# Performance work log

Hardware: AMD Instinct MI355X
Metric: run time of the kernel (lower is better)

## Reference

```python
import jax, jax.numpy as jnp
import numpy as np

NE = 200000   # num_entities
NR = 16       # num_relations
D  = 128      # embed_dim
B  = 4096     # batch
S  = 64       # neighbors per node
L  = 2        # num_layers
H  = 4        # attention heads (hardcoded in module)


def _ln(x, g, b, eps=1e-5):
    m = jnp.mean(x, -1, keepdims=True)
    v = jnp.mean((x - m) ** 2, -1, keepdims=True)
    return (x - m) * jax.lax.rsqrt(v + eps) * g + b


def setup_inputs() -> dict:
    key = jax.random.key(0)
    ks = jax.random.split(key, 12)
    s = 0.05
    return {
        'drug_entity_indices': jax.random.randint(ks[0], (B,), 0, NE),
        'adj_entity': jax.random.randint(ks[1], (B, S), 0, NE),
        'adj_relation': jax.random.randint(ks[2], (B, S), 0, NR),
        'edge_weights': jax.random.uniform(ks[3], (B, S), dtype=jnp.float32),
        'entity_emb': jax.random.normal(ks[4], (NE, D), jnp.float32) * s,
        'W_rgcn': jax.random.normal(ks[5], (L, NR, D, D), jnp.float32) * s,
        'res_w': jax.random.normal(ks[6], (L, D, D), jnp.float32) * s,
        'res_b': jnp.zeros((L, D), jnp.float32),
        'proj_w': jax.random.normal(ks[7], (L, D, D), jnp.float32) * s,
        'proj_b': jnp.zeros((L, D), jnp.float32),
        'ln_g': jnp.ones((L, D), jnp.float32),
        'ln_b': jnp.zeros((L, D), jnp.float32),
        'in_proj_w': jax.random.normal(ks[8], (3 * D, D), jnp.float32) * s,
        'in_proj_b': jnp.zeros((3 * D,), jnp.float32),
        'out_proj_w': jax.random.normal(ks[9], (D, D), jnp.float32) * s,
        'out_proj_b': jnp.zeros((D,), jnp.float32),
        'fln_g': jnp.ones((D,), jnp.float32),
        'fln_b': jnp.zeros((D,), jnp.float32),
    }


def reference(drug_entity_indices, adj_entity, adj_relation, edge_weights,
              entity_emb, W_rgcn, res_w, res_b, proj_w, proj_b, ln_g, ln_b,
              in_proj_w, in_proj_b, out_proj_w, out_proj_b, fln_g, fln_b):
    node = entity_emb[drug_entity_indices]           # [B,D] combined_emb
    nbr = entity_emb[adj_entity]                     # [B,S,D]
    # Route each edge to its relation: sum_s nbr*ew*[rel==r] then one GEMM per relation
    # (mathematically identical to the per-relation masked matmul loop in torch).
    onehot = jax.nn.one_hot(adj_relation, NR, dtype=node.dtype)      # [B,S,R]
    pre = jnp.einsum('bsd,bsr->brd', nbr * edge_weights[..., None], onehot)
    outs = []
    for l in range(L):
        msgs = jnp.einsum('brd,rde->be', pre, W_rgcn[l])             # [B,D]
        h = jax.nn.relu(node + msgs + node @ res_w[l].T + res_b[l])  # RGCNAggregator
        node = _ln(h @ proj_w[l].T + proj_b[l] + node, ln_g[l], ln_b[l])
        outs.append(node)
    x = jnp.stack(outs, 0)                           # [L,B,D] seq-first
    qkv = x @ in_proj_w.T + in_proj_b
    q, k, v = jnp.split(qkv, 3, axis=-1)
    hd = D // H
    def heads(t):
        return t.reshape(L, B, H, hd).transpose(1, 2, 0, 3)          # [B,H,L,hd]
    q, k, v = heads(q), heads(k), heads(v)
    att = jax.nn.softmax(jnp.einsum('bhld,bhmd->bhlm', q, k) / np.sqrt(hd).astype(np.float32), axis=-1)
    o = jnp.einsum('bhlm,bhmd->bhld', att, v).transpose(2, 0, 1, 3).reshape(L, B, D)
    o = o @ out_proj_w.T + out_proj_b
    return _ln(o.mean(0), fln_g, fln_b)              # [B,D]
```

## Files before the change

kernel.cpp:

```cpp
#include <hip/hip_runtime.h>
#include <math.h>

#define NRREL 16
#define DDIM 128
#define BBATCH 4096
#define SNBR 64
#define ROWS 16

typedef __attribute__((ext_vector_type(8))) short short8;
typedef __attribute__((ext_vector_type(4))) float floatx4;

__device__ __forceinline__ unsigned short f2bf(float f) {
    unsigned u = __builtin_bit_cast(unsigned, f);
    u += 0x7fffu + ((u >> 16) & 1u);
    return (unsigned short)(u >> 16);
}
__device__ __forceinline__ float bf2f(unsigned short u) {
    return __builtin_bit_cast(float, ((unsigned)u) << 16);
}

extern "C" __global__ __launch_bounds__(256)
void k_prep(const float* __restrict__ W_rgcn,
            const float* __restrict__ res_w, const float* __restrict__ proj_w,
            const float* __restrict__ in_w, const float* __restrict__ out_w,
            unsigned short* __restrict__ Wcat, unsigned short* __restrict__ resw,
            unsigned short* __restrict__ projw, unsigned short* __restrict__ inw,
            unsigned short* __restrict__ outw)
{
    __shared__ float tileT[64 * 65];
    const int bid = blockIdx.x, t = threadIdx.x;

    if (bid < 128) {
        const int l = bid >> 6, rem = bid & 63;
        const int k0 = (rem >> 1) * 64, e0 = (rem & 1) * 64;
        #pragma unroll
        for (int i = 0; i < 4; ++i) {
            int flat = t + 256 * i;
            int k = flat >> 4, c = flat & 15;
            float4 v = *(const float4*)(W_rgcn + ((size_t)(l * 2048 + k0 + k)) * 128 + e0 + 4 * c);
            tileT[(4 * c + 0) * 65 + k] = v.x;
            tileT[(4 * c + 1) * 65 + k] = v.y;
            tileT[(4 * c + 2) * 65 + k] = v.z;
            tileT[(4 * c + 3) * 65 + k] = v.w;
        }
        __syncthreads();
        const int e = t >> 2, m = t & 3;
        #pragma unroll
        for (int half = 0; half < 2; ++half) {
            int kk = 16 * m + 8 * half;
            short8 o;
            #pragma unroll
            for (int j = 0; j < 8; ++j) o[j] = (short)f2bf(tileT[e * 65 + kk + j]);
            *(short8*)(Wcat + ((size_t)(l * 128 + e0 + e)) * 2048 + k0 + kk) = o;
        }
    } else {
        int j4 = ((bid - 128) * 256 + t) * 4;
        const float* src; unsigned short* dst; int off;
        if (j4 < 32768)       { src = res_w;  dst = resw;  off = j4; }
        else if (j4 < 65536)  { src = proj_w; dst = projw; off = j4 - 32768; }
        else if (j4 < 114688) { src = in_w;   dst = inw;   off = j4 - 65536; }
        else                  { src = out_w;  dst = outw;  off = j4 - 114688; }
        float4 v = *(const float4*)(src + off);
        ushort4 o = { f2bf(v.x), f2bf(v.y), f2bf(v.z), f2bf(v.w) };
        *(ushort4*)(dst + off) = o;
    }
}

extern "C" __global__ __launch_bounds__(1024)
void k_fused(const int* __restrict__ drug, const int* __restrict__ adj_e,
             const int* __restrict__ adj_r, const float* __restrict__ ew,
             const float* __restrict__ emb,
             const unsigned short* __restrict__ Wcat,
             const unsigned short* __restrict__ resw, const unsigned short* __restrict__ projw,
             const float* __restrict__ res_b, const float* __restrict__ proj_b,
             const float* __restrict__ ln_g, const float* __restrict__ ln_b,
             const unsigned short* __restrict__ inw, const float* __restrict__ in_b,
             const unsigned short* __restrict__ outw, const float* __restrict__ out_b,
             const float* __restrict__ fg, const float* __restrict__ fb,
             float* __restrict__ outp)
{
    __shared__ union {
        struct { unsigned short preA[ROWS * 2056]; } a;
        struct {
            unsigned short h_b16[ROWS * 136];
            unsigned short xs_l[2 * ROWS * 136];
            unsigned short qkvl[2 * ROWS * 392];
        } t;
    } sm;
    __shared__ float node_ln[ROWS * 132];
    __shared__ unsigned short node_b16[ROWS * 136];
    __shared__ union {
        struct {
            int   cnt[ROWS][16];
            int   strt[ROWS][16];
            int   sperm[ROWS][64];
            float wperm[ROWS][64];
        } g;
        float msum[ROWS * 260];
    } sg;
    __shared__ float psum[16][16], psq[16][16];

    const int t = threadIdx.x, w = t >> 6, lane = t & 63, l15 = lane & 15, q = lane >> 4;
    const int r0 = blockIdx.x * ROWS;

    const int erow = t >> 6, es = t & 63;
    int   ent0 = adj_e[(r0 + erow) * SNBR + es];
    float ewt0 = ew[(r0 + erow) * SNBR + es];
    int   rel0 = adj_r[(r0 + erow) * SNBR + es];
    if (t < 256) sg.g.cnt[t >> 4][t & 15] = 0;
    if (t < 512) {
        int rr = t >> 5, c = t & 31;
        int di = drug[r0 + rr];
        float4 v = *(const float4*)(emb + (size_t)di * DDIM + 4 * c);
        *(float4*)(node_ln + rr * 132 + 4 * c) = v;
        ushort4 o = { f2bf(v.x), f2bf(v.y), f2bf(v.z), f2bf(v.w) };
        *(ushort4*)(node_b16 + rr * 136 + 4 * c) = o;
    }
    __syncthreads();

    atomicAdd(&sg.g.cnt[erow][rel0], 1);
    __syncthreads();

    if (t < ROWS) {
        int a = 0;
        #pragma unroll
        for (int r = 0; r < NRREL; ++r) { sg.g.strt[t][r] = a; a += sg.g.cnt[t][r]; }
    }
    __syncthreads();

    {
        int pos0 = atomicAdd(&sg.g.strt[erow][rel0], 1);
        sg.g.sperm[erow][pos0] = ent0;
        sg.g.wperm[erow][pos0] = ewt0;
    }
    __syncthreads();

    {
        #pragma unroll 1
        for (int i = 0; i < 4; ++i) {
            int u = t + 1024 * i;
            int row = u >> 8, rl = (u >> 4) & 15, g8 = u & 15;
            int n = sg.g.cnt[row][rl];
            int end = sg.g.strt[row][rl];
            int beg = end - n;
            float acc[8] = {0.f, 0.f, 0.f, 0.f, 0.f, 0.f, 0.f, 0.f};
            #pragma unroll 1
            for (int jb = beg; jb < end; jb += 8) {
                const float* pp[8]; float wq[8];
                #pragma unroll
                for (int u2 = 0; u2 < 8; ++u2) {
                    int live = (jb + u2 < end);
                    int j = live ? jb + u2 : beg;
                    wq[u2] = live ? sg.g.wperm[row][j] : 0.f;
                    pp[u2] = emb + (size_t)sg.g.sperm[row][j] * DDIM + 8 * g8;
                }
                float4 v0[8], v1[8];
                #pragma unroll
                for (int u2 = 0; u2 < 8; ++u2) {
                    v0[u2] = *(const float4*)pp[u2];
                    v1[u2] = *(const float4*)(pp[u2] + 4);
                }
                #pragma unroll
                for (int u2 = 0; u2 < 8; ++u2) {
                    acc[0] = fmaf(v0[u2].x, wq[u2], acc[0]); acc[1] = fmaf(v0[u2].y, wq[u2], acc[1]);
                    acc[2] = fmaf(v0[u2].z, wq[u2], acc[2]); acc[3] = fmaf(v0[u2].w, wq[u2], acc[3]);
                    acc[4] = fmaf(v1[u2].x, wq[u2], acc[4]); acc[5] = fmaf(v1[u2].y, wq[u2], acc[5]);
                    acc[6] = fmaf(v1[u2].z, wq[u2], acc[6]); acc[7] = fmaf(v1[u2].w, wq[u2], acc[7]);
                }
            }
            short8 o;
            #pragma unroll
            for (int jj = 0; jj < 8; ++jj) o[jj] = (short)f2bf(acc[jj]);
            *(short8*)(sm.a.preA + row * 2056 + rl * DDIM + 8 * g8) = o;
        }
    }
    __syncthreads();

    {
        floatx4 macc = {};
        const unsigned short* ap = sm.a.preA + l15 * 2056 + 8 * q;
        const unsigned short* bp = Wcat + (size_t)(16 * w + l15) * 2048 + 8 * q;
        #pragma unroll 8
        for (int k = 0; k < 2048; k += 32) {
            short8 A = *(const short8*)(ap + k);
            short8 B = *(const short8*)(bp + k);
            macc = __builtin_amdgcn_mfma_f32_16x16x32_bf16(A, B, macc, 0, 0, 0);
        }
        int gc = 16 * w + l15;
        #pragma unroll
        for (int r = 0; r < 4; ++r)
            sg.msum[(4 * q + r) * 260 + gc] = macc[r];
    }
    __syncthreads();

    for (int l = 0; l < 2; ++l) {
        if (w < 8) {
            const unsigned short* Bw = resw + (size_t)l * DDIM * DDIM;
            floatx4 acc = {};
            const unsigned short* ap = node_b16 + l15 * 136 + 8 * q;
            #pragma unroll
            for (int kk = 0; kk < DDIM; kk += 32) {
                short8 A = *(const short8*)(ap + kk);
                short8 B = *(const short8*)(Bw + (size_t)(16 * w + l15) * DDIM + kk + 8 * q);
                acc = __builtin_amdgcn_mfma_f32_16x16x32_bf16(A, B, acc, 0, 0, 0);
            }
            int gc = 16 * w + l15;
            float rb = res_b[l * DDIM + gc];
            #pragma unroll
            for (int r = 0; r < 4; ++r) {
                int lr = 4 * q + r;
                float v = acc[r] + rb + node_ln[lr * 132 + gc] + sg.msum[lr * 260 + l * DDIM + gc];
                sm.t.h_b16[lr * 136 + gc] = f2bf(v > 0.f ? v : 0.f);
            }
        }
        __syncthreads();
        {
            float vv[4];
            int gc = 16 * w + l15;
            if (w < 8) {
                const unsigned short* Bw = projw + (size_t)l * DDIM * DDIM;
                floatx4 acc = {};
                const unsigned short* ap = sm.t.h_b16 + l15 * 136 + 8 * q;
                #pragma unroll
                for (int kk = 0; kk < DDIM; kk += 32) {
                    short8 A = *(const short8*)(ap + kk);
                    short8 B = *(const short8*)(Bw + (size_t)(16 * w + l15) * DDIM + kk + 8 * q);
                    acc = __builtin_amdgcn_mfma_f32_16x16x32_bf16(A, B, acc, 0, 0, 0);
                }
                float s4[4], sq4[4];
                float pb = proj_b[l * DDIM + gc];
                #pragma unroll
                for (int r = 0; r < 4; ++r) {
                    float v = acc[r] + pb + node_ln[(4 * q + r) * 132 + gc];
                    vv[r] = v; s4[r] = v; sq4[r] = v * v;
                }
                #pragma unroll
                for (int r = 0; r < 4; ++r)
                    #pragma unroll
                    for (int off2 = 8; off2 >= 1; off2 >>= 1) {
                        s4[r] += __shfl_xor(s4[r], off2, 64);
                        sq4[r] += __shfl_xor(sq4[r], off2, 64);
                    }
                if (l15 == 0) {
                    #pragma unroll
                    for (int r = 0; r < 4; ++r) {
                        psum[w][4 * q + r] = s4[r];
                        psq[w][4 * q + r] = sq4[r];
                    }
                }
            }
            __syncthreads();
            if (w < 8) {
                float g2 = ln_g[l * DDIM + gc], bb = ln_b[l * DDIM + gc];
                #pragma unroll
                for (int r = 0; r < 4; ++r) {
                    int lr = 4 * q + r;
                    float ssum = 0.f, ssq = 0.f;
                    #pragma unroll
                    for (int ww = 0; ww < 8; ++ww) { ssum += psum[ww][lr]; ssq += psq[ww][lr]; }
                    float mean = ssum * (1.f / DDIM);
                    float var = ssq * (1.f / DDIM) - mean * mean;
                    float val = (vv[r] - mean) * rsqrtf(var + 1e-5f) * g2 + bb;
                    node_ln[lr * 132 + gc] = val;
                    unsigned short ub = f2bf(val);
                    node_b16[lr * 136 + gc] = ub;
                    sm.t.xs_l[(2 * lr + l) * 136 + gc] = ub;
                }
            }
            __syncthreads();
        }
    }

    if (w < 12) {
        floatx4 acc[4] = {};
        const unsigned short* ap = sm.t.xs_l + (16 * (w & 1) + l15) * 136 + 8 * q;
        #pragma unroll
        for (int kk = 0; kk < DDIM; kk += 32) {
            short8 A = *(const short8*)(ap + kk);
            #pragma unroll
            for (int ni = 0; ni < 4; ++ni) {
                short8 B = *(const short8*)(inw + (size_t)(64 * (w >> 1) + ni * 16 + l15) * DDIM + kk + 8 * q);
                acc[ni] = __builtin_amdgcn_mfma_f32_16x16x32_bf16(A, B, acc[ni], 0, 0, 0);
            }
        }
        #pragma unroll
        for (int ni = 0; ni < 4; ++ni) {
            int gc = 64 * (w >> 1) + ni * 16 + l15;
            float ib = in_b[gc];
            #pragma unroll
            for (int r = 0; r < 4; ++r)
                sm.t.qkvl[(16 * (w & 1) + 4 * q + r) * 392 + gc] = f2bf(acc[ni][r] + ib);
        }
    }
    __syncthreads();

    if (t < 128) {
        int g4 = t >> 3, j = t & 7;
        const unsigned short* row0 = sm.t.qkvl + (2 * g4) * 392;
        const unsigned short* row1 = row0 + 392;
        float p00 = 0.f, p01 = 0.f, p10 = 0.f, p11 = 0.f;
        #pragma unroll
        for (int dd = 0; dd < 16; ++dd) {
            int d = 16 * j + dd;
            float q0 = bf2f(row0[d]), k0 = bf2f(row0[128 + d]);
            float q1 = bf2f(row1[d]), k1 = bf2f(row1[128 + d]);
            p00 = fmaf(q0, k0, p00); p01 = fmaf(q0, k1, p01);
            p10 = fmaf(q1, k0, p10); p11 = fmaf(q1, k1, p11);
        }
        p00 += __shfl_xor(p00, 1, 64); p01 += __shfl_xor(p01, 1, 64);
        p10 += __shfl_xor(p10, 1, 64); p11 += __shfl_xor(p11, 1, 64);
        const float sc = 0.17677669529663687f;
        p00 *= sc; p01 *= sc; p10 *= sc; p11 *= sc;
        float m0 = fmaxf(p00, p01), e00 = expf(p00 - m0), e01 = expf(p01 - m0);
        float i0 = 1.f / (e00 + e01);
        float m1 = fmaxf(p10, p11), e10 = expf(p10 - m1), e11 = expf(p11 - m1);
        float i1 = 1.f / (e10 + e11);
        #pragma unroll
        for (int dd = 0; dd < 16; ++dd) {
            int d = 16 * j + dd;
            float v0 = bf2f(row0[256 + d]), v1 = bf2f(row1[256 + d]);
            sm.t.xs_l[(2 * g4) * 136 + d]     = f2bf((e00 * v0 + e01 * v1) * i0);
            sm.t.xs_l[(2 * g4 + 1) * 136 + d] = f2bf((e10 * v0 + e11 * v1) * i1);
        }
    }
    __syncthreads();

    {
        floatx4 acc = {};
        const unsigned short* ap = sm.t.xs_l + (16 * (w & 1) + l15) * 136 + 8 * q;
        #pragma unroll
        for (int kk = 0; kk < DDIM; kk += 32) {
            short8 A = *(const short8*)(ap + kk);
            short8 B = *(const short8*)(outw + (size_t)(16 * (w >> 1) + l15) * DDIM + kk + 8 * q);
            acc = __builtin_amdgcn_mfma_f32_16x16x32_bf16(A, B, acc, 0, 0, 0);
        }
        int gc = 16 * (w >> 1) + l15;
        float ob = out_b[gc];
        float av[2];
        float s2[2], sq2[2];
        #pragma unroll
        for (int rr = 0; rr < 2; ++rr) {
            float v = 0.5f * (acc[2 * rr] + acc[2 * rr + 1]) + ob;
            av[rr] = v; s2[rr] = v; sq2[rr] = v * v;
        }
        #pragma unroll
        for (int rr = 0; rr < 2; ++rr)
            #pragma unroll
            for (int off2 = 8; off2 >= 1; off2 >>= 1) {
                s2[rr] += __shfl_xor(s2[rr], off2, 64);
                sq2[rr] += __shfl_xor(sq2[rr], off2, 64);
            }
        if (l15 == 0) {
            #pragma unroll
            for (int rr = 0; rr < 2; ++rr) {
                psum[w][2 * q + rr] = s2[rr];
                psq[w][2 * q + rr] = sq2[rr];
            }
        }
        __syncthreads();
        float g2 = fg[gc], bb = fb[gc];
        #pragma unroll
        for (int rr = 0; rr < 2; ++rr) {
            int idx = 2 * q + rr;
            float ssum = 0.f, ssq = 0.f;
            #pragma unroll
            for (int ww = 0; ww < 8; ++ww) {
                ssum += psum[2 * ww + (w & 1)][idx];
                ssq  += psq[2 * ww + (w & 1)][idx];
            }
            float mean = ssum * (1.f / DDIM);
            float var = ssq * (1.f / DDIM) - mean * mean;
            outp[(size_t)(r0 + 8 * (w & 1) + idx) * DDIM + gc] =
                (av[rr] - mean) * rsqrtf(var + 1e-5f) * g2 + bb;
        }
    }
}

extern "C" void kernel_launch(void* const* d_in, const int* in_sizes, int n_in,
                              void* d_out, int out_size, void* d_ws, size_t ws_size,
                              hipStream_t stream) {
    const int*   drug_idx = (const int*)d_in[0];
    const int*   adj_ent  = (const int*)d_in[1];
    const int*   adj_rel  = (const int*)d_in[2];
    const float* ew       = (const float*)d_in[3];
    const float* emb      = (const float*)d_in[4];
    const float* W_rgcn   = (const float*)d_in[5];
    const float* res_w    = (const float*)d_in[6];
    const float* res_b    = (const float*)d_in[7];
    const float* proj_w   = (const float*)d_in[8];
    const float* proj_b   = (const float*)d_in[9];
    const float* ln_g     = (const float*)d_in[10];
    const float* ln_b     = (const float*)d_in[11];
    const float* in_w     = (const float*)d_in[12];
    const float* in_b     = (const float*)d_in[13];
    const float* out_w    = (const float*)d_in[14];
    const float* out_b    = (const float*)d_in[15];
    const float* fg       = (const float*)d_in[16];
    const float* fb       = (const float*)d_in[17];
    float* outp = (float*)d_out;

    char* ws = (char*)d_ws;
    size_t off = 0;
    auto alloc = [&](size_t bytes) { size_t o = off; off = (off + bytes + 255) & ~(size_t)255; return o; };
    unsigned short* Wcat    = (unsigned short*)(ws + alloc((size_t)256 * 2048 * 2));
    unsigned short* resw    = (unsigned short*)(ws + alloc((size_t)2 * 128 * 128 * 2));
    unsigned short* projw   = (unsigned short*)(ws + alloc((size_t)2 * 128 * 128 * 2));
    unsigned short* inw     = (unsigned short*)(ws + alloc((size_t)384 * 128 * 2));
    unsigned short* outw    = (unsigned short*)(ws + alloc((size_t)128 * 128 * 2));

    hipLaunchKernelGGL(k_prep, dim3(256), dim3(256), 0, stream,
                       W_rgcn, res_w, proj_w, in_w, out_w,
                       Wcat, resw, projw, inw, outw);
    hipLaunchKernelGGL(k_fused, dim3(BBATCH / ROWS), dim3(1024), 0, stream,
                       drug_idx, adj_ent, adj_rel, ew, emb,
                       Wcat, resw, projw, res_b, proj_b, ln_g, ln_b,
                       inw, in_b, outw, out_b, fg, fb, outp);
}
```

Measured before the change: 232.9 us.

## Restructure neighbor gather so one wave streams a row's sorted edges

The relation-bucketed gather is rebuilt. Previously each thread handled an 8-column slice of one (row, relation) bucket, with variable trip counts and 8-wide batches padded with dead loads. Now each wave owns one row and walks all 64 relation-sorted edges in order. Every lane loads a float2 of each neighbor, with software prefetch of the next 4, and resets its running sum whenever the relation changes. Partial sums are written to LDS at each step so the last write per relation wins, and empty relations are zeroed separately. This aims to remove load imbalance and divergent loops. The cost is narrower 8-byte loads per lane and many redundant LDS stores.

```diff
diff --git a/kernel.cpp b/kernel.cpp
--- a/kernel.cpp
+++ b/kernel.cpp
@@ -95,6 +95,7 @@
             int   strt[ROWS][16];
             int   sperm[ROWS][64];
             float wperm[ROWS][64];
+            int   relperm[ROWS][64];
         } g;
         float msum[ROWS * 260];
     } sg;
@@ -130,48 +131,85 @@
 
     {
         int pos0 = atomicAdd(&sg.g.strt[erow][rel0], 1);
-        sg.g.sperm[erow][pos0] = ent0;
-        sg.g.wperm[erow][pos0] = ewt0;
+        sg.g.sperm[erow][pos0]   = ent0;
+        sg.g.wperm[erow][pos0]   = ewt0;
+        sg.g.relperm[erow][pos0] = rel0;
     }
     __syncthreads();
 
     {
+        const int row = w;
+        if (t < 256) {
+            int rr = t >> 4, rl = t & 15;
+            if (sg.g.cnt[rr][rl] == 0) {
+                short8 z = {};
+                #pragma unroll
+                for (int ii = 0; ii < 16; ++ii)
+                    *(short8*)(sm.a.preA + rr * 2056 + rl * DDIM + 8 * ii) = z;
+            }
+        }
+        const float* embl = emb + 2 * lane;
+        unsigned short* prow = sm.a.preA + row * 2056 + 2 * lane;
+        float a0 = 0.f, a1 = 0.f;
+        int prev = -1;
+        int   e0 = sg.g.sperm[row][0], e1 = sg.g.sperm[row][1],
+              e2 = sg.g.sperm[row][2], e3 = sg.g.sperm[row][3];
+        float w0 = sg.g.wperm[row][0], w1 = sg.g.wperm[row][1],
+              w2 = sg.g.wperm[row][2], w3 = sg.g.wperm[row][3];
+        int   c0 = sg.g.relperm[row][0], c1 = sg.g.relperm[row][1],
+              c2 = sg.g.relperm[row][2], c3 = sg.g.relperm[row][3];
+        float2 v0 = *(const float2*)(embl + (size_t)e0 * DDIM);
+        float2 v1 = *(const float2*)(embl + (size_t)e1 * DDIM);
+        float2 v2 = *(const float2*)(embl + (size_t)e2 * DDIM);
+        float2 v3 = *(const float2*)(embl + (size_t)e3 * DDIM);
         #pragma unroll 1
-        for (int i = 0; i < 4; ++i) {
-            int u = t + 1024 * i;
-            int row = u >> 8, rl = (u >> 4) & 15, g8 = u & 15;
-            int n = sg.g.cnt[row][rl];
-            int end = sg.g.strt[row][rl];
-            int beg = end - n;
-            float acc[8] = {0.f, 0.f, 0.f, 0.f, 0.f, 0.f, 0.f, 0.f};
-            #pragma unroll 1
-            for (int jb = beg; jb < end; jb += 8) {
-                const float* pp[8]; float wq[8];
-                #pragma unroll
-                for (int u2 = 0; u2 < 8; ++u2) {
-                    int live = (jb + u2 < end);
-                    int j = live ? jb + u2 : beg;
-                    wq[u2] = live ? sg.g.wperm[row][j] : 0.f;
-                    pp[u2] = emb + (size_t)sg.g.sperm[row][j] * DDIM + 8 * g8;
-                }
-                float4 v0[8], v1[8];
-                #pragma unroll
-                for (int u2 = 0; u2 < 8; ++u2) {
-                    v0[u2] = *(const float4*)pp[u2];
-                    v1[u2] = *(const float4*)(pp[u2] + 4);
-                }
-                #pragma unroll
-                for (int u2 = 0; u2 < 8; ++u2) {
-                    acc[0] = fmaf(v0[u2].x, wq[u2], acc[0]); acc[1] = fmaf(v0[u2].y, wq[u2], acc[1]);
-                    acc[2] = fmaf(v0[u2].z, wq[u2], acc[2]); acc[3] = fmaf(v0[u2].w, wq[u2], acc[3]);
-                    acc[4] = fmaf(v1[u2].x, wq[u2], acc[4]); acc[5] = fmaf(v1[u2].y, wq[u2], acc[5]);
-                    acc[6] = fmaf(v1[u2].z, wq[u2], acc[6]); acc[7] = fmaf(v1[u2].w, wq[u2], acc[7]);
-                }
-            }
-            short8 o;
-            #pragma unroll
-            for (int jj = 0; jj < 8; ++jj) o[jj] = (short)f2bf(acc[jj]);
-            *(short8*)(sm.a.preA + row * 2056 + rl * DDIM + 8 * g8) = o;
+        for (int j = 0; j < SNBR; j += 4) {
+            float2 n0 = {}, n1 = {}, n2 = {}, n3 = {};
+            float nw0 = 0.f, nw1 = 0.f, nw2 = 0.f, nw3 = 0.f;
+            int nc0 = 0, nc1 = 0, nc2 = 0, nc3 = 0;
+            if (j + 4 < SNBR) {
+                int f0 = sg.g.sperm[row][j + 4], f1 = sg.g.sperm[row][j + 5],
+                    f2 = sg.g.sperm[row][j + 6], f3 = sg.g.sperm[row][j + 7];
+                nw0 = sg.g.wperm[row][j + 4]; nw1 = sg.g.wperm[row][j + 5];
+                nw2 = sg.g.wperm[row][j + 6]; nw3 = sg.g.wperm[row][j + 7];
+                nc0 = sg.g.relperm[row][j + 4]; nc1 = sg.g.relperm[row][j + 5];
+                nc2 = sg.g.relperm[row][j + 6]; nc3 = sg.g.relperm[row][j + 7];
+                n0 = *(const float2*)(embl + (size_t)f0 * DDIM);
+                n1 = *(const float2*)(embl + (size_t)f1 * DDIM);
+                n2 = *(const float2*)(embl + (size_t)f2 * DDIM);
+                n3 = *(const float2*)(embl + (size_t)f3 * DDIM);
+            }
+            {
+                bool ch = (c0 != prev);
+                a0 = ch ? 0.f : a0; a1 = ch ? 0.f : a1;
+                a0 = fmaf(v0.x, w0, a0); a1 = fmaf(v0.y, w0, a1);
+                unsigned pk = (unsigned)f2bf(a0) | ((unsigned)f2bf(a1) << 16);
+                *(unsigned*)(prow + (size_t)c0 * DDIM) = pk; prev = c0;
+            }
+            {
+                bool ch = (c1 != prev);
+                a0 = ch ? 0.f : a0; a1 = ch ? 0.f : a1;
+                a0 = fmaf(v1.x, w1, a0); a1 = fmaf(v1.y, w1, a1);
+                unsigned pk = (unsigned)f2bf(a0) | ((unsigned)f2bf(a1) << 16);
+                *(unsigned*)(prow + (size_t)c1 * DDIM) = pk; prev = c1;
+            }
+            {
+                bool ch = (c2 != prev);
+                a0 = ch ? 0.f : a0; a1 = ch ? 0.f : a1;
+                a0 = fmaf(v2.x, w2, a0); a1 = fmaf(v2.y, w2, a1);
+                unsigned pk = (unsigned)f2bf(a0) | ((unsigned)f2bf(a1) << 16);
+                *(unsigned*)(prow + (size_t)c2 * DDIM) = pk; prev = c2;
+            }
+            {
+                bool ch = (c3 != prev);
+                a0 = ch ? 0.f : a0; a1 = ch ? 0.f : a1;
+                a0 = fmaf(v3.x, w3, a0); a1 = fmaf(v3.y, w3, a1);
+                unsigned pk = (unsigned)f2bf(a0) | ((unsigned)f2bf(a1) << 16);
+                *(unsigned*)(prow + (size_t)c3 * DDIM) = pk; prev = c3;
+            }
+            v0 = n0; v1 = n1; v2 = n2; v3 = n3;
+            w0 = nw0; w1 = nw1; w2 = nw2; w3 = nw3;
+            c0 = nc0; c1 = nc1; c2 = nc2; c3 = nc3;
         }
     }
     __syncthreads();
```

Measured after the change: 230.7 us, median of 2. No clear change (-1.0%).
